# Performance work log

Measured on AMD Instinct MI355X. Metric: run time of the kernel, lower is better.

The kernel has to match this reference:

```python
import jax, jax.numpy as jnp
import numpy as np

LN_EPS = 1e-5  # torch nn.LayerNorm default
L2_EPS = 1e-12  # F.normalize default


def layer_norm(x, gamma, beta):
    mu = jnp.mean(x, axis=-1, keepdims=True)
    var = jnp.mean(jnp.square(x - mu), axis=-1, keepdims=True)
    return (x - mu) * jax.lax.rsqrt(var + LN_EPS) * gamma + beta


def l2_normalize(x):
    n = jnp.linalg.norm(x, axis=-1, keepdims=True)
    return x / jnp.maximum(n, L2_EPS)


def setup_inputs() -> dict:
    key = jax.random.key(0)
    k_x, k_mu = jax.random.split(key, 2)
    B, C, H, W = 4, 512, 128, 128
    K, M = 19, 5  # num_classes, num_components_per_class
    x = jax.random.normal(k_x, (B, C, H, W), dtype=jnp.float32)
    means = 0.02 * jax.random.normal(k_mu, (K, M, C), dtype=jnp.float32)  # trunc_normal_(std=0.02)
    diagonal = jnp.ones((K, M, C), dtype=jnp.float32)
    feat_gamma = jnp.ones((C,), dtype=jnp.float32)
    feat_beta = jnp.zeros((C,), dtype=jnp.float32)
    mask_gamma = jnp.ones((K,), dtype=jnp.float32)
    mask_beta = jnp.zeros((K,), dtype=jnp.float32)
    return dict(x=x, means=means, diagonal=diagonal,
                feat_gamma=feat_gamma, feat_beta=feat_beta,
                mask_gamma=mask_gamma, mask_beta=mask_beta)


def reference(x, means, diagonal, feat_gamma, feat_beta, mask_gamma, mask_beta):
    B, C, H, W = x.shape
    K, M, D = means.shape
    # rearrange 'b c h w -> (b h w) c'
    f = jnp.transpose(x, (0, 2, 3, 1)).reshape(-1, C)  # (N, D)
    f = layer_norm(f, feat_gamma, feat_beta)
    f = l2_normalize(f)
    # means are re-normalized in-place each forward
    mu = l2_normalize(means).reshape(K * M, D)          # (P, D), P = K*M
    sigma = diagonal.reshape(K * M, D)                  # diagonal scale (std)
    inv_var = 1.0 / jnp.square(sigma)
    # Mahalanobis distance via quadratic expansion (avoids (N,P,D) intermediate):
    # sum_d ((f - mu)/sigma)^2 = f^2 . iv - 2 f . (mu*iv) + sum(mu^2 * iv)
    q1 = jnp.square(f) @ inv_var.T                      # (N, P)
    q2 = f @ (mu * inv_var).T                           # (N, P)
    q3 = jnp.sum(jnp.square(mu) * inv_var, axis=-1)     # (P,)
    maha = q1 - 2.0 * q2 + q3[None, :]
    log_det = jnp.sum(jnp.log(sigma), axis=-1)          # sum log sigma, (P,)
    half_log2pi = 0.5 * D * jnp.log(2.0 * jnp.pi)
    log_prob = -0.5 * maha - log_det[None, :] - half_log2pi  # (N, P)
    log_prob = log_prob.reshape(-1, K, M)
    m_prob = jnp.max(log_prob, axis=-1)                 # amax over components, (N, K)
    out = layer_norm(m_prob, mask_gamma, mask_beta)
    # rearrange '(b h w) k -> b k h w'
    out_seg = jnp.transpose(out.reshape(B, H, W, K), (0, 3, 1, 2))
    return out_seg
```

## Files before the change

### kernel.cpp

```cpp
#include <hip/hip_runtime.h>
#include <math.h>

#define C_ 512
#define HW_ 16384
#define K_ 19
#define M_ 5
#define P_ 95
#define P2 96
#define TPX 32
#define NBLK 2048
#define HL2PI 470.49652900081467f

typedef __attribute__((ext_vector_type(8))) short short8;
typedef __attribute__((ext_vector_type(4))) float float4v;

static __device__ __forceinline__ short f2bf(float f) {
  unsigned u = __builtin_bit_cast(unsigned, f);
  unsigned r = (u + 0x7fffu + ((u >> 16) & 1u)) >> 16;
  return (short)r;
}

__device__ __forceinline__ float block_reduce_sum(float v, volatile float* red) {
#pragma unroll
  for (int o = 32; o; o >>= 1) v += __shfl_down(v, o);
  const int lane = threadIdx.x & 63, wv = threadIdx.x >> 6;
  if (lane == 0) red[wv] = v;
  __syncthreads();
  float r = red[0] + red[1] + red[2] + red[3];
  __syncthreads();
  return r;
}

__global__ __launch_bounds__(256) void prep_kernel(
    const float* __restrict__ means, const float* __restrict__ diag,
    short* __restrict__ wbf, float* __restrict__ cterm) {
  const int p = blockIdx.x;
  const int tid = threadIdx.x;
  __shared__ float red[4];
  if (p >= P_) {
    for (int c = tid; c < C_; c += 256) {
      wbf[p * 1024 + c] = 0;
      wbf[p * 1024 + 512 + c] = 0;
    }
    if (tid == 0) cterm[p] = 0.f;
    return;
  }
  const float* mrow = means + (size_t)p * C_;
  const float* srow = diag + (size_t)p * C_;
  float m0 = mrow[tid], m1 = mrow[tid + 256];
  float ss = block_reduce_sum(m0 * m0 + m1 * m1, red);
  float rden = 1.f / fmaxf(sqrtf(ss), 1e-12f);
  float q3 = 0.f, ld = 0.f;
#pragma unroll
  for (int t = 0; t < 2; t++) {
    int c = tid + t * 256;
    float m = mrow[c], s = srow[c];
    float mu = m * rden;
    float iv = 1.f / (s * s);
    wbf[p * 1024 + c] = f2bf(iv);
    wbf[p * 1024 + 512 + c] = f2bf(mu * iv);
    q3 += mu * mu * iv;
    ld += logf(s);
  }
  q3 = block_reduce_sum(q3, red);
  ld = block_reduce_sum(ld, red);
  if (tid == 0) cterm[p] = -0.5f * q3 - ld - HL2PI;
}

__global__ __launch_bounds__(256) void main_kernel(
    const float* __restrict__ x,
    const float* __restrict__ fg, const float* __restrict__ fb,
    const float* __restrict__ mg, const float* __restrict__ mb,
    const short* __restrict__ wbf, const float* __restrict__ cterm,
    float* __restrict__ out) {
  __shared__ __align__(16) char raw[65536];
  __shared__ float red0[8 * TPX], red1[8 * TPX];
  __shared__ float meanA[TPX], rstdA[TPX], rnA[TPX], rn2A[TPX];
  __shared__ float mean2A[TPX], rstd2A[TPX];
  __shared__ float mpr[TPX * 20];

  const int tid = threadIdx.x;
  const int px = tid & 31, part = tid >> 5;
  const int n0 = blockIdx.x * TPX;
  const int b = n0 >> 14;
  const int rem = n0 & 16383;
  const int h = rem >> 7;
  const int w0 = rem & 127;

  const float* xp = x + (size_t)b * C_ * HW_ + h * 128 + w0 + px;
  const int cbase = part * 64;
  float xr[64];
#pragma unroll
  for (int i = 0; i < 64; i++) xr[i] = xp[(size_t)(cbase + i) * HW_];
  {
    float s = 0.f, q = 0.f;
#pragma unroll
    for (int i = 0; i < 64; i++) {
      s += xr[i];
      q += xr[i] * xr[i];
    }
    red0[part * 32 + px] = s;
    red1[part * 32 + px] = q;
  }
  __syncthreads();
  if (tid < 32) {
    float ss = 0.f, qq = 0.f;
#pragma unroll
    for (int i = 0; i < 8; i++) {
      ss += red0[i * 32 + tid];
      qq += red1[i * 32 + tid];
    }
    float mean = ss * (1.f / C_);
    float var = qq * (1.f / C_) - mean * mean;
    meanA[tid] = mean;
    rstdA[tid] = rsqrtf(var + 1e-5f);
  }
  __syncthreads();

  {
    const float mean = meanA[px], rstd = rstdA[px];
    float s2 = 0.f;
    const int t_ = px >> 4;
    const int lq = px & 15;
#pragma unroll
    for (int t8 = 0; t8 < 8; t8++) {
      const int c0 = cbase + t8 * 8;
      short8 v2p, vp;
#pragma unroll
      for (int j = 0; j < 8; j++) {
        const int c = c0 + j;
        float v = (xr[t8 * 8 + j] - mean) * rstd;
        v = fmaf(v, fg[c], fb[c]);
        s2 += v * v;
        v2p[j] = f2bf(v * v);
        vp[j] = f2bf(v);
      }
      const int l = (((c0 >> 3) & 3) << 4) | lq;
      const int ks1 = c0 >> 5;
      const int ks2 = 16 + ks1;
      *(short8*)(raw + (((t_ * 32 + ks1) << 10) | (l << 4))) = v2p;
      *(short8*)(raw + (((t_ * 32 + ks2) << 10) | (l << 4))) = vp;
    }
    red0[part * 32 + px] = s2;
  }
  __syncthreads();
  if (tid < 32) {
    float ss = 0.f;
#pragma unroll
    for (int i = 0; i < 8; i++) ss += red0[i * 32 + tid];
    float rn = 1.f / fmaxf(sqrtf(ss), 1e-12f);
    rnA[tid] = rn;
    rn2A[tid] = rn * rn;
  }
  __syncthreads();

  const int wv = tid >> 6, lane = tid & 63;
  const int pbase = (wv & 1) * 3;
  const int khalf = wv >> 1;
  const int lm = lane & 15, lk = lane >> 4;
  float4v acc[3][2] = {};
  const short* wrow = wbf + (((pbase * 16 + lm) << 10) | (khalf << 9) | (lk << 3));
#pragma unroll 4
  for (int ksl = 0; ksl < 16; ksl++) {
    const int ks = khalf * 16 + ksl;
    short8 a0 = *(const short8*)(wrow + ksl * 32);
    short8 a1 = *(const short8*)(wrow + 16384 + ksl * 32);
    short8 a2 = *(const short8*)(wrow + 32768 + ksl * 32);
    short8 b0 = *(const short8*)(raw + ((ks << 10) | (lane << 4)));
    short8 b1 = *(const short8*)(raw + (((32 + ks) << 10) | (lane << 4)));
    acc[0][0] = __builtin_amdgcn_mfma_f32_16x16x32_bf16(a0, b0, acc[0][0], 0, 0, 0);
    acc[0][1] = __builtin_amdgcn_mfma_f32_16x16x32_bf16(a0, b1, acc[0][1], 0, 0, 0);
    acc[1][0] = __builtin_amdgcn_mfma_f32_16x16x32_bf16(a1, b0, acc[1][0], 0, 0, 0);
    acc[1][1] = __builtin_amdgcn_mfma_f32_16x16x32_bf16(a1, b1, acc[1][1], 0, 0, 0);
    acc[2][0] = __builtin_amdgcn_mfma_f32_16x16x32_bf16(a2, b0, acc[2][0], 0, 0, 0);
    acc[2][1] = __builtin_amdgcn_mfma_f32_16x16x32_bf16(a2, b1, acc[2][1], 0, 0, 0);
  }
  __syncthreads();
  float* lp = (float*)raw;

  if (khalf == 0) {
#pragma unroll
    for (int i = 0; i < 3; i++) {
      const int prow = (pbase + i) * 16 + lk * 4;
#pragma unroll
      for (int r = 0; r < 4; r++) {
        const float ct = cterm[prow + r];
#pragma unroll
        for (int t = 0; t < 2; t++) {
          const int pxx = t * 16 + lm;
          lp[pxx * 100 + prow + r] = fmaf(-0.5f * rn2A[pxx], acc[i][t][r], ct);
        }
      }
    }
  }
  __syncthreads();
  if (khalf == 1) {
#pragma unroll
    for (int i = 0; i < 3; i++) {
      const int prow = (pbase + i) * 16 + lk * 4;
#pragma unroll
      for (int r = 0; r < 4; r++) {
#pragma unroll
        for (int t = 0; t < 2; t++) {
          const int pxx = t * 16 + lm;
          lp[pxx * 100 + prow + r] += rnA[pxx] * acc[i][t][r];
        }
      }
    }
  }
  __syncthreads();

  for (int idx = tid; idx < TPX * K_; idx += 256) {
    const int pxx = idx / K_;
    const int k = idx - pxx * K_;
    const float* row = lp + pxx * 100 + k * M_;
    float mv = row[0];
#pragma unroll
    for (int m = 1; m < M_; m++) mv = fmaxf(mv, row[m]);
    mpr[pxx * 20 + k] = mv;
  }
  __syncthreads();
  if (tid < 32) {
    float ss = 0.f;
    for (int k = 0; k < K_; k++) ss += mpr[tid * 20 + k];
    float m2 = ss * (1.f / K_);
    float qq = 0.f;
    for (int k = 0; k < K_; k++) {
      float d = mpr[tid * 20 + k] - m2;
      qq += d * d;
    }
    mean2A[tid] = m2;
    rstd2A[tid] = rsqrtf(qq * (1.f / K_) + 1e-5f);
  }
  __syncthreads();
  float* obase = out + ((size_t)(b * K_) * 128 + h) * 128 + w0;
  for (int idx = tid; idx < TPX * K_; idx += 256) {
    const int k = idx >> 5, pxx = idx & 31;
    float v = fmaf((mpr[pxx * 20 + k] - mean2A[pxx]) * rstd2A[pxx], mg[k], mb[k]);
    obase[(size_t)k * HW_ + pxx] = v;
  }
}

extern "C" void kernel_launch(void* const* d_in, const int* in_sizes, int n_in,
                              void* d_out, int out_size, void* d_ws, size_t ws_size,
                              hipStream_t stream) {
  const float* x = (const float*)d_in[0];
  const float* means = (const float*)d_in[1];
  const float* diag = (const float*)d_in[2];
  const float* fg = (const float*)d_in[3];
  const float* fb = (const float*)d_in[4];
  const float* mg = (const float*)d_in[5];
  const float* mb = (const float*)d_in[6];
  float* out = (float*)d_out;

  short* wbf = (short*)d_ws;
  float* cterm = (float*)((char*)d_ws + (size_t)P2 * 1024 * 2);

  prep_kernel<<<P2, 256, 0, stream>>>(means, diag, wbf, cterm);
  main_kernel<<<NBLK, 256, 0, stream>>>(x, fg, fb, mg, mb, wbf, cterm, out);
}
```

Before: 81.45 us.

## Fold LayerNorm affine and L2 norm algebraically into GEMM weights on raw x

```diff
diff --git a/kernel.cpp b/kernel.cpp
--- a/kernel.cpp
+++ b/kernel.cpp
@@ -12,6 +12,7 @@
 #define HL2PI 470.49652900081467f
 
 typedef __attribute__((ext_vector_type(8))) short short8;
+typedef __attribute__((ext_vector_type(4))) int int4v;
 typedef __attribute__((ext_vector_type(4))) float float4v;
 
 static __device__ __forceinline__ short f2bf(float f) {
@@ -20,6 +21,25 @@
   return (short)r;
 }
 
+static __device__ __forceinline__ int pk2(float a, float b) {
+  int r;
+  asm("v_cvt_pk_bf16_f32 %0, %1, %2" : "=v"(r) : "v"(a), "v"(b));
+  return r;
+}
+
+static __device__ __forceinline__ short8 sq8(short8 a) {
+  int4v ai = __builtin_bit_cast(int4v, a);
+  int4v ri;
+#pragma unroll
+  for (int j = 0; j < 4; j++) {
+    unsigned u = (unsigned)ai[j];
+    float lo = __builtin_bit_cast(float, u << 16);
+    float hi = __builtin_bit_cast(float, u & 0xffff0000u);
+    ri[j] = pk2(lo * lo, hi * hi);
+  }
+  return __builtin_bit_cast(short8, ri);
+}
+
 __device__ __forceinline__ float block_reduce_sum(float v, volatile float* red) {
 #pragma unroll
   for (int o = 32; o; o >>= 1) v += __shfl_down(v, o);
@@ -33,16 +53,35 @@
 
 __global__ __launch_bounds__(256) void prep_kernel(
     const float* __restrict__ means, const float* __restrict__ diag,
-    short* __restrict__ wbf, float* __restrict__ cterm) {
+    const float* __restrict__ fg, const float* __restrict__ fb,
+    short* __restrict__ wbf, float* __restrict__ ctp) {
   const int p = blockIdx.x;
   const int tid = threadIdx.x;
   __shared__ float red[4];
-  if (p >= P_) {
-    for (int c = tid; c < C_; c += 256) {
-      wbf[p * 1024 + c] = 0;
-      wbf[p * 1024 + 512 + c] = 0;
-    }
-    if (tid == 0) cterm[p] = 0.f;
+  if (p == P_) {
+    float t1 = 0.f, t2 = 0.f, t3 = 0.f;
+#pragma unroll
+    for (int t = 0; t < 2; t++) {
+      int c = tid + t * 256;
+      float g = fg[c], bb = fb[c];
+      wbf[p * 1536 + c] = f2bf(g * g);
+      wbf[p * 1536 + 512 + c] = f2bf(g * bb);
+      wbf[p * 1536 + 1024 + c] = f2bf(g);
+      t1 += bb * bb;
+      t2 += g * bb;
+      t3 += g * g;
+    }
+    t1 = block_reduce_sum(t1, red);
+    t2 = block_reduce_sum(t2, red);
+    t3 = block_reduce_sum(t3, red);
+    if (tid == 0) {
+      ctp[p * 8 + 0] = 0.f;
+      ctp[p * 8 + 1] = t1;
+      ctp[p * 8 + 2] = t2;
+      ctp[p * 8 + 3] = t3;
+      ctp[p * 8 + 4] = 0.f;
+      ctp[p * 8 + 5] = 0.f;
+    }
     return;
   }
   const float* mrow = means + (size_t)p * C_;
@@ -50,57 +89,84 @@
   float m0 = mrow[tid], m1 = mrow[tid + 256];
   float ss = block_reduce_sum(m0 * m0 + m1 * m1, red);
   float rden = 1.f / fmaxf(sqrtf(ss), 1e-12f);
-  float q3 = 0.f, ld = 0.f;
+  float t1 = 0.f, t2 = 0.f, t3 = 0.f, t4 = 0.f, t5 = 0.f, q3 = 0.f, ld = 0.f;
 #pragma unroll
   for (int t = 0; t < 2; t++) {
     int c = tid + t * 256;
-    float m = mrow[c], s = srow[c];
+    float m = mrow[c], sg = srow[c], g = fg[c], bb = fb[c];
     float mu = m * rden;
-    float iv = 1.f / (s * s);
-    wbf[p * 1024 + c] = f2bf(iv);
-    wbf[p * 1024 + 512 + c] = f2bf(mu * iv);
+    float iv = 1.f / (sg * sg);
+    wbf[p * 1536 + c] = f2bf(iv * g * g);
+    wbf[p * 1536 + 512 + c] = f2bf(iv * g * bb);
+    wbf[p * 1536 + 1024 + c] = f2bf(mu * iv * g);
+    t1 += iv * bb * bb;
+    t2 += iv * g * bb;
+    t3 += iv * g * g;
+    t4 += mu * iv * bb;
+    t5 += mu * iv * g;
     q3 += mu * mu * iv;
-    ld += logf(s);
-  }
+    ld += logf(sg);
+  }
+  t1 = block_reduce_sum(t1, red);
+  t2 = block_reduce_sum(t2, red);
+  t3 = block_reduce_sum(t3, red);
+  t4 = block_reduce_sum(t4, red);
+  t5 = block_reduce_sum(t5, red);
   q3 = block_reduce_sum(q3, red);
   ld = block_reduce_sum(ld, red);
-  if (tid == 0) cterm[p] = -0.5f * q3 - ld - HL2PI;
-}
-
-__global__ __launch_bounds__(256) void main_kernel(
+  if (tid == 0) {
+    ctp[p * 8 + 0] = -0.5f * q3 - ld - HL2PI;
+    ctp[p * 8 + 1] = t1;
+    ctp[p * 8 + 2] = t2;
+    ctp[p * 8 + 3] = t3;
+    ctp[p * 8 + 4] = t4;
+    ctp[p * 8 + 5] = t5;
+  }
+}
+
+__global__ __launch_bounds__(256, 4) void main_kernel(
     const float* __restrict__ x,
-    const float* __restrict__ fg, const float* __restrict__ fb,
+    const short* __restrict__ wbf, const float* __restrict__ ctp,
     const float* __restrict__ mg, const float* __restrict__ mb,
-    const short* __restrict__ wbf, const float* __restrict__ cterm,
     float* __restrict__ out) {
-  __shared__ __align__(16) char raw[65536];
-  __shared__ float red0[8 * TPX], red1[8 * TPX];
-  __shared__ float meanA[TPX], rstdA[TPX], rnA[TPX], rn2A[TPX];
+  __shared__ __align__(16) char raw[32768];
+  __shared__ float red0[256], red1[256];
+  __shared__ float meanA[TPX], rstdA[TPX], rnA[TPX];
   __shared__ float mean2A[TPX], rstd2A[TPX];
   __shared__ float mpr[TPX * 20];
 
   const int tid = threadIdx.x;
   const int px = tid & 31, part = tid >> 5;
+  const int wv = tid >> 6, lane = tid & 63;
   const int n0 = blockIdx.x * TPX;
   const int b = n0 >> 14;
   const int rem = n0 & 16383;
   const int h = rem >> 7;
   const int w0 = rem & 127;
-
+  const int cbase = part * 64;
+  const int t_ = px >> 4, lq = px & 15;
   const float* xp = x + (size_t)b * C_ * HW_ + h * 128 + w0 + px;
-  const int cbase = part * 64;
-  float xr[64];
-#pragma unroll
-  for (int i = 0; i < 64; i++) xr[i] = xp[(size_t)(cbase + i) * HW_];
+
+  float xv[64];
+#pragma unroll
+  for (int i = 0; i < 64; i++) xv[i] = xp[(size_t)(cbase + i) * HW_];
   {
-    float s = 0.f, q = 0.f;
-#pragma unroll
-    for (int i = 0; i < 64; i++) {
-      s += xr[i];
-      q += xr[i] * xr[i];
-    }
-    red0[part * 32 + px] = s;
-    red1[part * 32 + px] = q;
+    float s1 = 0.f, s2 = 0.f;
+#pragma unroll
+    for (int g = 0; g < 8; g++) {
+      const int c0 = cbase + g * 8;
+      int4v pk;
+#pragma unroll
+      for (int j2 = 0; j2 < 4; j2++) {
+        float a = xv[g * 8 + 2 * j2], bb = xv[g * 8 + 2 * j2 + 1];
+        s1 += a + bb;
+        s2 = fmaf(a, a, fmaf(bb, bb, s2));
+        pk[j2] = pk2(a, bb);
+      }
+      *(int4v*)(raw + (((t_ * 16 + (c0 >> 5)) << 10) | (((((c0 >> 3) & 3) << 4) | lq) << 4))) = pk;
+    }
+    red0[part * 32 + px] = s1;
+    red1[part * 32 + px] = s2;
   }
   __syncthreads();
   if (tid < 32) {
@@ -117,94 +183,66 @@
   }
   __syncthreads();
 
-  {
-    const float mean = meanA[px], rstd = rstdA[px];
-    float s2 = 0.f;
-    const int t_ = px >> 4;
-    const int lq = px & 15;
-#pragma unroll
-    for (int t8 = 0; t8 < 8; t8++) {
-      const int c0 = cbase + t8 * 8;
-      short8 v2p, vp;
-#pragma unroll
-      for (int j = 0; j < 8; j++) {
-        const int c = c0 + j;
-        float v = (xr[t8 * 8 + j] - mean) * rstd;
-        v = fmaf(v, fg[c], fb[c]);
-        s2 += v * v;
-        v2p[j] = f2bf(v * v);
-        vp[j] = f2bf(v);
-      }
-      const int l = (((c0 >> 3) & 3) << 4) | lq;
-      const int ks1 = c0 >> 5;
-      const int ks2 = 16 + ks1;
-      *(short8*)(raw + (((t_ * 32 + ks1) << 10) | (l << 4))) = v2p;
-      *(short8*)(raw + (((t_ * 32 + ks2) << 10) | (l << 4))) = vp;
-    }
-    red0[part * 32 + px] = s2;
-  }
-  __syncthreads();
-  if (tid < 32) {
-    float ss = 0.f;
-#pragma unroll
-    for (int i = 0; i < 8; i++) ss += red0[i * 32 + tid];
-    float rn = 1.f / fmaxf(sqrtf(ss), 1e-12f);
-    rnA[tid] = rn;
-    rn2A[tid] = rn * rn;
-  }
-  __syncthreads();
-
-  const int wv = tid >> 6, lane = tid & 63;
   const int pbase = (wv & 1) * 3;
-  const int khalf = wv >> 1;
+  const int pxt = wv >> 1;
   const int lm = lane & 15, lk = lane >> 4;
-  float4v acc[3][2] = {};
-  const short* wrow = wbf + (((pbase * 16 + lm) << 10) | (khalf << 9) | (lk << 3));
+  float4v a1[3] = {}, a2[3] = {}, a3[3] = {}, a4[3] = {};
+  const short* wA = wbf + ((pbase * 16 + lm) * 1536 + lk * 8);
+  const short* wB = wbf + (((pbase + 1) * 16 + lm) * 1536 + lk * 8);
+  const short* wC = wbf + (((pbase + 2) * 16 + lm) * 1536 + lk * 8);
 #pragma unroll 4
   for (int ksl = 0; ksl < 16; ksl++) {
-    const int ks = khalf * 16 + ksl;
-    short8 a0 = *(const short8*)(wrow + ksl * 32);
-    short8 a1 = *(const short8*)(wrow + 16384 + ksl * 32);
-    short8 a2 = *(const short8*)(wrow + 32768 + ksl * 32);
-    short8 b0 = *(const short8*)(raw + ((ks << 10) | (lane << 4)));
-    short8 b1 = *(const short8*)(raw + (((32 + ks) << 10) | (lane << 4)));
-    acc[0][0] = __builtin_amdgcn_mfma_f32_16x16x32_bf16(a0, b0, acc[0][0], 0, 0, 0);
-    acc[0][1] = __builtin_amdgcn_mfma_f32_16x16x32_bf16(a0, b1, acc[0][1], 0, 0, 0);
-    acc[1][0] = __builtin_amdgcn_mfma_f32_16x16x32_bf16(a1, b0, acc[1][0], 0, 0, 0);
-    acc[1][1] = __builtin_amdgcn_mfma_f32_16x16x32_bf16(a1, b1, acc[1][1], 0, 0, 0);
-    acc[2][0] = __builtin_amdgcn_mfma_f32_16x16x32_bf16(a2, b0, acc[2][0], 0, 0, 0);
-    acc[2][1] = __builtin_amdgcn_mfma_f32_16x16x32_bf16(a2, b1, acc[2][1], 0, 0, 0);
+    short8 bx = *(const short8*)(raw + pxt * 16384 + (ksl << 10) + (lane << 4));
+    short8 bx2 = sq8(bx);
+    short8 sA0 = *(const short8*)(wA + ksl * 32);
+    short8 sA1 = *(const short8*)(wA + 512 + ksl * 32);
+    short8 sA2 = *(const short8*)(wA + 1024 + ksl * 32);
+    a1[0] = __builtin_amdgcn_mfma_f32_16x16x32_bf16(sA0, bx2, a1[0], 0, 0, 0);
+    a2[0] = __builtin_amdgcn_mfma_f32_16x16x32_bf16(sA0, bx, a2[0], 0, 0, 0);
+    a3[0] = __builtin_amdgcn_mfma_f32_16x16x32_bf16(sA1, bx, a3[0], 0, 0, 0);
+    a4[0] = __builtin_amdgcn_mfma_f32_16x16x32_bf16(sA2, bx, a4[0], 0, 0, 0);
+    short8 sB0 = *(const short8*)(wB + ksl * 32);
+    short8 sB1 = *(const short8*)(wB + 512 + ksl * 32);
+    short8 sB2 = *(const short8*)(wB + 1024 + ksl * 32);
+    a1[1] = __builtin_amdgcn_mfma_f32_16x16x32_bf16(sB0, bx2, a1[1], 0, 0, 0);
+    a2[1] = __builtin_amdgcn_mfma_f32_16x16x32_bf16(sB0, bx, a2[1], 0, 0, 0);
+    a3[1] = __builtin_amdgcn_mfma_f32_16x16x32_bf16(sB1, bx, a3[1], 0, 0, 0);
+    a4[1] = __builtin_amdgcn_mfma_f32_16x16x32_bf16(sB2, bx, a4[1], 0, 0, 0);
+    short8 sC0 = *(const short8*)(wC + ksl * 32);
+    short8 sC1 = *(const short8*)(wC + 512 + ksl * 32);
+    short8 sC2 = *(const short8*)(wC + 1024 + ksl * 32);
+    a1[2] = __builtin_amdgcn_mfma_f32_16x16x32_bf16(sC0, bx2, a1[2], 0, 0, 0);
+    a2[2] = __builtin_amdgcn_mfma_f32_16x16x32_bf16(sC0, bx, a2[2], 0, 0, 0);
+    a3[2] = __builtin_amdgcn_mfma_f32_16x16x32_bf16(sC1, bx, a3[2], 0, 0, 0);
+    a4[2] = __builtin_amdgcn_mfma_f32_16x16x32_bf16(sC2, bx, a4[2], 0, 0, 0);
+  }
+
+  if ((wv & 1) == 1 && lk == 3) {
+    const int pxx = pxt * 16 + lm;
+    float mu_ = meanA[pxx], s_ = rstdA[pxx];
+    float ms = mu_ * s_;
+    float T1 = ctp[95 * 8 + 1], T2 = ctp[95 * 8 + 2], T3 = ctp[95 * 8 + 3];
+    float sv = s_ * s_ * a1[2][3] + 2.f * s_ * a3[2][3] - 2.f * ms * s_ * a2[2][3] +
+               (T1 - 2.f * ms * T2 + ms * ms * T3);
+    rnA[pxx] = 1.f / fmaxf(sqrtf(sv), 1e-12f);
   }
   __syncthreads();
   float* lp = (float*)raw;
 
-  if (khalf == 0) {
+  {
+    const int pxx = pxt * 16 + lm;
+    const float mu_ = meanA[pxx], s_ = rstdA[pxx], rn = rnA[pxx];
+    const float ms = mu_ * s_, ss = s_ * s_, Ac = -0.5f * rn * rn;
 #pragma unroll
     for (int i = 0; i < 3; i++) {
-      const int prow = (pbase + i) * 16 + lk * 4;
 #pragma unroll
       for (int r = 0; r < 4; r++) {
-        const float ct = cterm[prow + r];
-#pragma unroll
-        for (int t = 0; t < 2; t++) {
-          const int pxx = t * 16 + lm;
-          lp[pxx * 100 + prow + r] = fmaf(-0.5f * rn2A[pxx], acc[i][t][r], ct);
-        }
-      }
-    }
-  }
-  __syncthreads();
-  if (khalf == 1) {
-#pragma unroll
-    for (int i = 0; i < 3; i++) {
-      const int prow = (pbase + i) * 16 + lk * 4;
-#pragma unroll
-      for (int r = 0; r < 4; r++) {
-#pragma unroll
-        for (int t = 0; t < 2; t++) {
-          const int pxx = t * 16 + lm;
-          lp[pxx * 100 + prow + r] += rnA[pxx] * acc[i][t][r];
-        }
+        const int p = (pbase + i) * 16 + lk * 4 + r;
+        const float* c6 = ctp + p * 8;
+        float q1 = ss * a1[i][r] + 2.f * s_ * a3[i][r] - 2.f * ms * s_ * a2[i][r] +
+                   (c6[1] - 2.f * ms * c6[2] + ms * ms * c6[3]);
+        float q2 = s_ * a4[i][r] + c6[4] - ms * c6[5];
+        lp[pxx * 100 + p] = fmaf(Ac, q1, fmaf(rn, q2, c6[0]));
       }
     }
   }
@@ -254,8 +292,8 @@
   float* out = (float*)d_out;
 
   short* wbf = (short*)d_ws;
-  float* cterm = (float*)((char*)d_ws + (size_t)P2 * 1024 * 2);
-
-  prep_kernel<<<P2, 256, 0, stream>>>(means, diag, wbf, cterm);
-  main_kernel<<<NBLK, 256, 0, stream>>>(x, fg, fb, mg, mb, wbf, cterm, out);
-}
+  float* ctp = (float*)((char*)d_ws + (size_t)P2 * 1536 * 2);
+
+  prep_kernel<<<P2, 256, 0, stream>>>(means, diag, fg, fb, wbf, ctp);
+  main_kernel<<<NBLK, 256, 0, stream>>>(x, wbf, ctp, mg, mb, out);
+}
```

Result: slower. 153.9 us (+89.0%).
